# Kernel optimization log

Measured on AMD Instinct MI355X. Metric: run time of the kernel, lower is better.

Reference implementation:

```python
import jax, jax.numpy as jnp
import numpy as np
import math

N, E, B, T = 100000, 500000, 4096, 12
IN, HID, H = 64, 32, 4
HC = HID * H  # 128
ED = 4


def setup_inputs() -> dict:
    key = jax.random.key(0)
    ks = jax.random.split(key, 40)
    w = lambda k, shape: jax.random.normal(k, shape, jnp.float32) * 0.05
    inp = {
        'x': jax.random.normal(ks[0], (N, IN), jnp.float32),
        'edge_index': jax.random.randint(ks[1], (2, E), 0, N, jnp.int32),
        'edge_attr': jax.random.normal(ks[2], (E, ED), jnp.float32),
        'batch': jnp.sort(jax.random.randint(ks[3], (N,), 0, B, jnp.int32)),
        'r_target': jax.random.randint(ks[4], (B,), 0, T, jnp.int32),
        # layer 1 (in=IN)
        'Wq1': w(ks[5], (IN, HC)), 'bq1': w(ks[6], (HC,)),
        'Wk1': w(ks[7], (IN, HC)), 'bk1': w(ks[8], (HC,)),
        'Wv1': w(ks[9], (IN, HC)), 'bv1': w(ks[10], (HC,)),
        'We1': w(ks[11], (ED, HC)),
        'Ws1': w(ks[12], (IN, HC)), 'bs1': w(ks[13], (HC,)),
        # layers 2 and 3 stacked (in=HC)
        'Wq23': w(ks[14], (2, HC, HC)), 'bq23': w(ks[15], (2, HC)),
        'Wk23': w(ks[16], (2, HC, HC)), 'bk23': w(ks[17], (2, HC)),
        'Wv23': w(ks[18], (2, HC, HC)), 'bv23': w(ks[19], (2, HC)),
        'We23': w(ks[20], (2, ED, HC)),
        'Ws23': w(ks[21], (2, HC, HC)), 'bs23': w(ks[22], (2, HC)),
        # per-task linear heads (out_channels=1)
        'head_W': w(ks[23], (T, HC)), 'head_b': w(ks[24], (T,)),
    }
    return inp


def tconv(x, src, dst, ea, Wq, bq, Wk, bk, Wv, bv, We, Ws, bs):
    """PyG TransformerConv: gather -> per-edge MHA score -> segment softmax -> scatter."""
    q = (x @ Wq + bq).reshape(-1, H, HID)   # [N,H,C]
    k = (x @ Wk + bk).reshape(-1, H, HID)
    v = (x @ Wv + bv).reshape(-1, H, HID)
    e = (ea @ We).reshape(-1, H, HID)       # [E,H,C] (lin_edge has no bias)
    kj = k[src] + e                          # [E,H,C]
    alpha = (q[dst] * kj).sum(-1) / math.sqrt(HID)          # [E,H]
    amax = jax.ops.segment_max(alpha, dst, num_segments=N)  # [N,H]
    alpha = jnp.exp(alpha - amax[dst])
    asum = jax.ops.segment_sum(alpha, dst, num_segments=N)
    alpha = alpha / (asum[dst] + 1e-16)
    msg = (v[src] + e) * alpha[..., None]                   # [E,H,C]
    out = jax.ops.segment_sum(msg, dst, num_segments=N).reshape(N, HC)
    return out + x @ Ws + bs                 # root_weight skip connection


def reference(x, edge_index, edge_attr, batch, r_target,
              Wq1, bq1, Wk1, bk1, Wv1, bv1, We1, Ws1, bs1,
              Wq23, bq23, Wk23, bk23, Wv23, bv23, We23, Ws23, bs23,
              head_W, head_b):
    src, dst = edge_index[0], edge_index[1]
    h = jax.nn.relu(tconv(x, src, dst, edge_attr, Wq1, bq1, Wk1, bk1, Wv1, bv1, We1, Ws1, bs1))
    h = jax.nn.relu(tconv(h, src, dst, edge_attr, Wq23[0], bq23[0], Wk23[0], bk23[0], Wv23[0], bv23[0], We23[0], Ws23[0], bs23[0]))
    h = tconv(h, src, dst, edge_attr, Wq23[1], bq23[1], Wk23[1], bk23[1], Wv23[1], bv23[1], We23[1], Ws23[1], bs23[1])
    # global mean pool per graph
    cnt = jax.ops.segment_sum(jnp.ones((N,), h.dtype), batch, num_segments=B)
    pooled = jax.ops.segment_sum(h, batch, num_segments=B) / jnp.maximum(cnt, 1.0)[:, None]  # [B,HC]
    # dropout p=0.3 is a no-op in eval mode
    # per-task head selected by r_target (out_channels=1, squeezed)
    return (pooled * head_W[r_target]).sum(-1) + head_b[r_target]  # [B]
```

## Files before the change

kernel.cpp:

```cpp
#include <hip/hip_runtime.h>
#include <hip/hip_bf16.h>

#define NN 100000
#define EE 500000
#define BB 4096
#define HC 128
#define SCAN_ELEM 1024
#define NSB ((NN + SCAN_ELEM - 1) / SCAN_ELEM)

typedef __bf16 bf16_t;
typedef bf16_t bf16x8 __attribute__((ext_vector_type(8)));
typedef float f32x4 __attribute__((ext_vector_type(4)));

__device__ __forceinline__ unsigned short f2bf(float f) {
    unsigned u = __builtin_bit_cast(unsigned, f);
    u += 0x7FFFu + ((u >> 16) & 1u);
    return (unsigned short)(u >> 16);
}
__device__ __forceinline__ float bflo(unsigned u) {
    return __builtin_bit_cast(float, u << 16);
}
__device__ __forceinline__ float bfhi(unsigned u) {
    return __builtin_bit_cast(float, u & 0xFFFF0000u);
}

__global__ __launch_bounds__(256) void conv_x(const float* __restrict__ in,
                                              unsigned short* __restrict__ outb,
                                              int total4)
{
    const int g = blockIdx.x * 256 + threadIdx.x;
    if (g >= total4) return;
    const float4 f = *(const float4*)(in + (size_t)g * 4);
    ushort4 u;
    u.x = f2bf(f.x); u.y = f2bf(f.y); u.z = f2bf(f.z); u.w = f2bf(f.w);
    *(ushort4*)(outb + (size_t)g * 4) = u;
}

__global__ __launch_bounds__(256) void prep_w(
    const float* __restrict__ Wq, const float* __restrict__ Wk,
    const float* __restrict__ Wv, const float* __restrict__ Ws,
    unsigned short* __restrict__ Wt, int K)
{
    const int g = blockIdx.x * 256 + threadIdx.x;
    const int per = K * 128;
    if (g >= 4 * per) return;
    const int p = g / per, r = g - p * per;
    const int k = r >> 7, n = r & 127;
    const float* W = p == 0 ? Wq : p == 1 ? Wk : p == 2 ? Wv : Ws;
    Wt[(size_t)p * per + (size_t)n * K + k] = f2bf(W[k * 128 + n]);
}

template<int NKT>
__global__ __launch_bounds__(256) void gemm_mfma(
    const unsigned short* __restrict__ A,
    const unsigned short* __restrict__ Wt,
    const float* __restrict__ bq, const float* __restrict__ bk,
    const float* __restrict__ bv, const float* __restrict__ bs,
    unsigned* __restrict__ Qb, unsigned* __restrict__ Kb,
    unsigned* __restrict__ Vb, unsigned* __restrict__ Sb)
{
    constexpr int K = NKT * 32;
    const int lane = threadIdx.x & 63;
    const int p = threadIdx.x >> 6;
    const int m = lane & 15, kq = lane >> 4;
    const int rows0 = blockIdx.x * 32;

    const unsigned short* Wp = Wt + (size_t)p * 128 * K;
    const float* bias = p == 0 ? bq : p == 1 ? bk : p == 2 ? bv : bs;
    unsigned* out = p == 0 ? Qb : p == 1 ? Kb : p == 2 ? Vb : Sb;

    bf16x8 a[2][NKT];
#pragma unroll
    for (int mt = 0; mt < 2; mt++)
#pragma unroll
        for (int kt = 0; kt < NKT; kt++)
            a[mt][kt] = *(const bf16x8*)(A + (size_t)(rows0 + mt * 16 + m) * K + kt * 32 + kq * 8);

    f32x4 acc[2][8];
#pragma unroll
    for (int mt = 0; mt < 2; mt++)
#pragma unroll
        for (int nt = 0; nt < 8; nt++)
            acc[mt][nt] = (f32x4){0.f, 0.f, 0.f, 0.f};

#pragma unroll
    for (int nt = 0; nt < 8; nt++) {
#pragma unroll
        for (int kt = 0; kt < NKT; kt++) {
            const bf16x8 b = *(const bf16x8*)(Wp + (size_t)(nt * 16 + m) * K + kt * 32 + kq * 8);
            acc[0][nt] = __builtin_amdgcn_mfma_f32_16x16x32_bf16(a[0][kt], b, acc[0][nt], 0, 0, 0);
            acc[1][nt] = __builtin_amdgcn_mfma_f32_16x16x32_bf16(a[1][kt], b, acc[1][nt], 0, 0, 0);
        }
    }

#pragma unroll
    for (int nt = 0; nt < 8; nt++) {
        const float bi = bias[nt * 16 + m];
#pragma unroll
        for (int mt = 0; mt < 2; mt++) {
#pragma unroll
            for (int r = 0; r < 4; r++) {
                const float v0 = acc[mt][nt][r] + bi;
                const float v1 = __shfl_xor(v0, 1);
                if (!(m & 1)) {
                    const unsigned pk = (unsigned)f2bf(v0) | ((unsigned)f2bf(v1) << 16);
                    out[(size_t)(rows0 + mt * 16 + kq * 4 + r) * 64 + nt * 8 + (m >> 1)] = pk;
                }
            }
        }
    }
}

__global__ __launch_bounds__(256) void deg_k(const int* __restrict__ ei, int* __restrict__ deg)
{
    const int e = blockIdx.x * 256 + threadIdx.x;
    if (e < EE) atomicAdd(&deg[ei[EE + e]], 1);
}

__global__ __launch_bounds__(256) void scan_part(const int* __restrict__ deg,
                                                 int* __restrict__ bsum)
{
    __shared__ int red[256];
    const int base = blockIdx.x * SCAN_ELEM + threadIdx.x * 4;
    int s = 0;
#pragma unroll
    for (int j = 0; j < 4; j++) { const int i = base + j; if (i < NN) s += deg[i]; }
    red[threadIdx.x] = s;
    __syncthreads();
    for (int st = 128; st > 0; st >>= 1) {
        if (threadIdx.x < st) red[threadIdx.x] += red[threadIdx.x + st];
        __syncthreads();
    }
    if (threadIdx.x == 0) bsum[blockIdx.x] = red[0];
}

__global__ __launch_bounds__(128) void scan_top(const int* __restrict__ bsum,
                                                int* __restrict__ boff)
{
    __shared__ int buf[128];
    const int v = (threadIdx.x < NSB) ? bsum[threadIdx.x] : 0;
    buf[threadIdx.x] = v;
    __syncthreads();
    for (int s = 1; s < 128; s <<= 1) {
        const int t = (threadIdx.x >= s) ? buf[threadIdx.x - s] : 0;
        __syncthreads();
        buf[threadIdx.x] += t;
        __syncthreads();
    }
    if (threadIdx.x < NSB) boff[threadIdx.x] = buf[threadIdx.x] - v;
}

__global__ __launch_bounds__(256) void scan_final(const int* __restrict__ deg,
                                                  const int* __restrict__ boff,
                                                  int* __restrict__ off,
                                                  int* __restrict__ cursor)
{
    __shared__ int tsum[256];
    const int base = blockIdx.x * SCAN_ELEM + threadIdx.x * 4;
    int vals[4];
    int s = 0;
#pragma unroll
    for (int j = 0; j < 4; j++) {
        const int i = base + j;
        vals[j] = (i < NN) ? deg[i] : 0;
        s += vals[j];
    }
    tsum[threadIdx.x] = s;
    __syncthreads();
    for (int st = 1; st < 256; st <<= 1) {
        const int t = (threadIdx.x >= st) ? tsum[threadIdx.x - st] : 0;
        __syncthreads();
        tsum[threadIdx.x] += t;
        __syncthreads();
    }
    int ex = boff[blockIdx.x] + tsum[threadIdx.x] - s;
#pragma unroll
    for (int j = 0; j < 4; j++) {
        const int i = base + j;
        if (i < NN) { off[i] = ex; cursor[i] = ex; }
        ex += vals[j];
    }
    if (blockIdx.x == NSB - 1 && threadIdx.x == 255)
        off[NN] = boff[blockIdx.x] + tsum[255];
}

__global__ __launch_bounds__(256) void bucket_k(const int* __restrict__ ei,
                                                const float* __restrict__ ea,
                                                int* __restrict__ cursor,
                                                int* __restrict__ esrc,
                                                float4* __restrict__ eaf)
{
    const int e = blockIdx.x * 256 + threadIdx.x;
    if (e < EE) {
        const int d = ei[EE + e];
        const int p = atomicAdd(&cursor[d], 1);
        esrc[p] = ei[e];
        eaf[p] = *(const float4*)(ea + (size_t)e * 4);
    }
}

__global__ __launch_bounds__(256) void cnt_k(const int* __restrict__ batch,
                                             float* __restrict__ cnt)
{
    const int n = blockIdx.x * 256 + threadIdx.x;
    if (n < NN) atomicAdd(&cnt[batch[n]], 1.0f);
}

__global__ __launch_bounds__(256) void edge_fused(
    const int* __restrict__ esrc, const float4* __restrict__ eaf,
    const float* __restrict__ We,
    const unsigned* __restrict__ Qb, const unsigned* __restrict__ Kb,
    const unsigned* __restrict__ Vb,
    const int* __restrict__ off, const unsigned* __restrict__ Sb,
    unsigned short* __restrict__ Hb,
    const int* __restrict__ batch, float* __restrict__ pooled,
    int fuse_pool)
{
    __shared__ float wes[512];
    for (int i = threadIdx.x; i < 512; i += 256) wes[i] = We[i];
    __syncthreads();

    const int lane = threadIdx.x & 63;
    const int n = blockIdx.x * 4 + (threadIdx.x >> 6);
    const int c = lane * 2;
    const float w00 = wes[c],     w10 = wes[128 + c],     w20 = wes[256 + c],     w30 = wes[384 + c];
    const float w01 = wes[c + 1], w11 = wes[128 + c + 1], w21 = wes[256 + c + 1], w31 = wes[384 + c + 1];

    const int beg = off[n], end = off[n + 1];
    const unsigned qu = Qb[(size_t)n * 64 + lane];
    const float q0 = bflo(qu), q1 = bfhi(qu);
    float num0 = 0.f, num1 = 0.f, den = 0.f;

    int src = 0;
    float4 a4 = make_float4(0.f, 0.f, 0.f, 0.f);
    if (beg < end) { src = esrc[beg]; a4 = eaf[beg]; }

    for (int p = beg; p < end; p++) {
        const unsigned ku = Kb[(size_t)src * 64 + lane];
        const unsigned vu = Vb[(size_t)src * 64 + lane];
        const float4 ac = a4;
        if (p + 1 < end) { src = esrc[p + 1]; a4 = eaf[p + 1]; }
        const float e0 = ac.x * w00 + ac.y * w10 + ac.z * w20 + ac.w * w30;
        const float e1 = ac.x * w01 + ac.y * w11 + ac.z * w21 + ac.w * w31;
        float part = q0 * (bflo(ku) + e0) + q1 * (bfhi(ku) + e1);
        part += __shfl_xor(part, 1);
        part += __shfl_xor(part, 2);
        part += __shfl_xor(part, 4);
        part += __shfl_xor(part, 8);
        const float al = expf(part * 0.17677669529663687f);
        num0 += (bflo(vu) + e0) * al;
        num1 += (bfhi(vu) + e1) * al;
        den += al;
    }

    const unsigned su = Sb[(size_t)n * 64 + lane];
    const float inv = 1.f / (den + 1e-16f);
    float o0 = num0 * inv + bflo(su);
    float o1 = num1 * inv + bfhi(su);
    if (!fuse_pool) {
        o0 = fmaxf(o0, 0.f);
        o1 = fmaxf(o1, 0.f);
        const unsigned pk = (unsigned)f2bf(o0) | ((unsigned)f2bf(o1) << 16);
        *(unsigned*)(Hb + (size_t)n * HC + c) = pk;
    } else {
        const int b = batch[n];
        atomicAdd(pooled + (size_t)b * HC + c, o0);
        atomicAdd(pooled + (size_t)b * HC + c + 1, o1);
    }
}

__global__ __launch_bounds__(256) void head_k(
    const float* __restrict__ pooled, const float* __restrict__ cnt,
    const int* __restrict__ rt, const float* __restrict__ hW,
    const float* __restrict__ hb, float* __restrict__ out)
{
    const int lane = threadIdx.x & 63;
    const int b = blockIdx.x * 4 + (threadIdx.x >> 6);
    if (b >= BB) return;
    const int t = rt[b];
    const int c = lane * 2;
    const float2 p2 = *(const float2*)(pooled + (size_t)b * HC + c);
    const float2 w2 = *(const float2*)(hW + (size_t)t * HC + c);
    float part = p2.x * w2.x + p2.y * w2.y;
    part += __shfl_xor(part, 1);
    part += __shfl_xor(part, 2);
    part += __shfl_xor(part, 4);
    part += __shfl_xor(part, 8);
    part += __shfl_xor(part, 16);
    part += __shfl_xor(part, 32);
    if (lane == 0) out[b] = part / fmaxf(cnt[b], 1.0f) + hb[t];
}

extern "C" void kernel_launch(void* const* d_in, const int* in_sizes, int n_in,
                              void* d_out, int out_size, void* d_ws, size_t ws_size,
                              hipStream_t stream) {
    const float* x      = (const float*)d_in[0];
    const int*   ei     = (const int*)d_in[1];
    const float* ea     = (const float*)d_in[2];
    const int*   batch  = (const int*)d_in[3];
    const int*   rt     = (const int*)d_in[4];

    unsigned* Qb  = (unsigned*)d_ws;
    unsigned* Kb  = Qb + 6400000;
    unsigned* Vb  = Kb + 6400000;
    unsigned* Sb  = Vb + 6400000;
    unsigned short* Abf = (unsigned short*)(Sb + 6400000);
    float4* eaf   = (float4*)(Abf + 12800000);
    unsigned short* Wt = (unsigned short*)(eaf + 500000);
    float* pooled = (float*)(Wt + 65536);
    float* cnt    = pooled + 524288;
    int*   esrc   = (int*)(cnt + 4096);
    int*   deg    = esrc + 500000;
    int*   off    = deg + 100000;
    int*   cursor = off + 100004;
    int*   bsum   = cursor + 100000;
    int*   boff   = bsum + 128;

    hipMemsetAsync(deg, 0, 100000 * sizeof(int), stream);
    deg_k<<<(EE + 255) / 256, 256, 0, stream>>>(ei, deg);
    scan_part<<<NSB, 256, 0, stream>>>(deg, bsum);
    scan_top<<<1, 128, 0, stream>>>(bsum, boff);
    scan_final<<<NSB, 256, 0, stream>>>(deg, boff, off, cursor);
    bucket_k<<<(EE + 255) / 256, 256, 0, stream>>>(ei, ea, cursor, esrc, eaf);

    hipMemsetAsync(pooled, 0, (size_t)(BB * HC + BB) * sizeof(float), stream);
    cnt_k<<<(NN + 255) / 256, 256, 0, stream>>>(batch, cnt);

    conv_x<<<(NN * 64 / 4 + 255) / 256, 256, 0, stream>>>(x, Abf, NN * 64 / 4);

    for (int l = 0; l < 3; l++) {
        const int K = (l == 0) ? 64 : 128;
        const float *Wq, *Wk, *Wv, *Wsk, *bq, *bk, *bv, *bs, *We;
        if (l == 0) {
            Wq = (const float*)d_in[5];  bq = (const float*)d_in[6];
            Wk = (const float*)d_in[7];  bk = (const float*)d_in[8];
            Wv = (const float*)d_in[9];  bv = (const float*)d_in[10];
            We = (const float*)d_in[11];
            Wsk= (const float*)d_in[12]; bs = (const float*)d_in[13];
        } else {
            const int j = l - 1;
            Wq = (const float*)d_in[14] + (size_t)j * HC * HC;  bq = (const float*)d_in[15] + j * HC;
            Wk = (const float*)d_in[16] + (size_t)j * HC * HC;  bk = (const float*)d_in[17] + j * HC;
            Wv = (const float*)d_in[18] + (size_t)j * HC * HC;  bv = (const float*)d_in[19] + j * HC;
            We = (const float*)d_in[20] + (size_t)j * 4 * HC;
            Wsk= (const float*)d_in[21] + (size_t)j * HC * HC;  bs = (const float*)d_in[22] + j * HC;
        }

        prep_w<<<(4 * K * 128 + 255) / 256, 256, 0, stream>>>(Wq, Wk, Wv, Wsk, Wt, K);
        if (K == 64)
            gemm_mfma<2><<<NN / 32, 256, 0, stream>>>(Abf, Wt, bq, bk, bv, bs, Qb, Kb, Vb, Sb);
        else
            gemm_mfma<4><<<NN / 32, 256, 0, stream>>>(Abf, Wt, bq, bk, bv, bs, Qb, Kb, Vb, Sb);
        edge_fused<<<NN / 4, 256, 0, stream>>>(esrc, eaf, We, Qb, Kb, Vb, off,
                                               Sb, Abf, batch, pooled,
                                               l == 2 ? 1 : 0);
    }

    head_k<<<BB / 4, 256, 0, stream>>>(pooled, cnt, rt,
        (const float*)d_in[23], (const float*)d_in[24], (float*)d_out);
}
```

Baseline: 689.7 us.

## Sort nodes by in-degree so edge kernel waves get balanced work

Adds a degree histogram, scan and scatter that build a per-node record (node id, edge begin, edge end), with nodes grouped by in-degree capped at 32. The edge aggregation kernel now reads its node from this degree-sorted list instead of taking nodes in index order. The aim is for the four wavefronts in a block to have similar edge counts, which cuts idle time and divergence from degree imbalance. The cost is three extra small kernels, and node ordering within each degree bin comes from atomics, so memory locality for Q loads and output writes gets worse.

```diff
diff --git a/kernel.cpp b/kernel.cpp
--- a/kernel.cpp
+++ b/kernel.cpp
@@ -199,6 +199,43 @@
     }
 }
 
+__global__ __launch_bounds__(256) void dhist_k(const int* __restrict__ deg,
+                                               int* __restrict__ hist)
+{
+    const int n = blockIdx.x * 256 + threadIdx.x;
+    if (n < NN) atomicAdd(&hist[min(deg[n], 32)], 1);
+}
+
+__global__ __launch_bounds__(64) void dscan_k(int* __restrict__ hist,
+                                              int* __restrict__ hcur)
+{
+    __shared__ int buf[64];
+    const int v = (threadIdx.x < 33) ? hist[threadIdx.x] : 0;
+    buf[threadIdx.x] = v;
+    __syncthreads();
+    for (int s = 1; s < 64; s <<= 1) {
+        const int t = (threadIdx.x >= s) ? buf[threadIdx.x - s] : 0;
+        __syncthreads();
+        buf[threadIdx.x] += t;
+        __syncthreads();
+    }
+    if (threadIdx.x < 33) hcur[threadIdx.x] = buf[threadIdx.x] - v;
+}
+
+__global__ __launch_bounds__(256) void dscat_k(const int* __restrict__ deg,
+                                               const int* __restrict__ off,
+                                               int* __restrict__ hcur,
+                                               int4* __restrict__ nodeinfo)
+{
+    const int n = blockIdx.x * 256 + threadIdx.x;
+    if (n < NN) {
+        const int d = deg[n];
+        const int p = atomicAdd(&hcur[min(d, 32)], 1);
+        const int b = off[n];
+        nodeinfo[p] = make_int4(n, b, b + d, 0);
+    }
+}
+
 __global__ __launch_bounds__(256) void cnt_k(const int* __restrict__ batch,
                                              float* __restrict__ cnt)
 {
@@ -211,7 +248,7 @@
     const float* __restrict__ We,
     const unsigned* __restrict__ Qb, const unsigned* __restrict__ Kb,
     const unsigned* __restrict__ Vb,
-    const int* __restrict__ off, const unsigned* __restrict__ Sb,
+    const int4* __restrict__ nodeinfo, const unsigned* __restrict__ Sb,
     unsigned short* __restrict__ Hb,
     const int* __restrict__ batch, float* __restrict__ pooled,
     int fuse_pool)
@@ -221,12 +258,12 @@
     __syncthreads();
 
     const int lane = threadIdx.x & 63;
-    const int n = blockIdx.x * 4 + (threadIdx.x >> 6);
+    const int4 ni = nodeinfo[blockIdx.x * 4 + (threadIdx.x >> 6)];
+    const int n = ni.x, beg = ni.y, end = ni.z;
     const int c = lane * 2;
     const float w00 = wes[c],     w10 = wes[128 + c],     w20 = wes[256 + c],     w30 = wes[384 + c];
     const float w01 = wes[c + 1], w11 = wes[128 + c + 1], w21 = wes[256 + c + 1], w31 = wes[384 + c + 1];
 
-    const int beg = off[n], end = off[n + 1];
     const unsigned qu = Qb[(size_t)n * 64 + lane];
     const float q0 = bflo(qu), q1 = bfhi(qu);
     float num0 = 0.f, num1 = 0.f, den = 0.f;
@@ -306,22 +343,29 @@
     unsigned* Sb  = Vb + 6400000;
     unsigned short* Abf = (unsigned short*)(Sb + 6400000);
     float4* eaf   = (float4*)(Abf + 12800000);
-    unsigned short* Wt = (unsigned short*)(eaf + 500000);
+    int4* nodeinfo= (int4*)(eaf + 500000);
+    unsigned short* Wt = (unsigned short*)(nodeinfo + 100000);
     float* pooled = (float*)(Wt + 65536);
     float* cnt    = pooled + 524288;
     int*   esrc   = (int*)(cnt + 4096);
     int*   deg    = esrc + 500000;
-    int*   off    = deg + 100000;
+    int*   hist   = deg + 100000;
+    int*   hcur   = hist + 64;
+    int*   off    = hcur + 64;
     int*   cursor = off + 100004;
     int*   bsum   = cursor + 100000;
     int*   boff   = bsum + 128;
 
-    hipMemsetAsync(deg, 0, 100000 * sizeof(int), stream);
+    hipMemsetAsync(deg, 0, (100000 + 64) * sizeof(int), stream);
     deg_k<<<(EE + 255) / 256, 256, 0, stream>>>(ei, deg);
     scan_part<<<NSB, 256, 0, stream>>>(deg, bsum);
     scan_top<<<1, 128, 0, stream>>>(bsum, boff);
     scan_final<<<NSB, 256, 0, stream>>>(deg, boff, off, cursor);
     bucket_k<<<(EE + 255) / 256, 256, 0, stream>>>(ei, ea, cursor, esrc, eaf);
+
+    dhist_k<<<(NN + 255) / 256, 256, 0, stream>>>(deg, hist);
+    dscan_k<<<1, 64, 0, stream>>>(hist, hcur);
+    dscat_k<<<(NN + 255) / 256, 256, 0, stream>>>(deg, off, hcur, nodeinfo);
 
     hipMemsetAsync(pooled, 0, (size_t)(BB * HC + BB) * sizeof(float), stream);
     cnt_k<<<(NN + 255) / 256, 256, 0, stream>>>(batch, cnt);
@@ -351,7 +395,7 @@
             gemm_mfma<2><<<NN / 32, 256, 0, stream>>>(Abf, Wt, bq, bk, bv, bs, Qb, Kb, Vb, Sb);
         else
             gemm_mfma<4><<<NN / 32, 256, 0, stream>>>(Abf, Wt, bq, bk, bv, bs, Qb, Kb, Vb, Sb);
-        edge_fused<<<NN / 4, 256, 0, stream>>>(esrc, eaf, We, Qb, Kb, Vb, off,
+        edge_fused<<<NN / 4, 256, 0, stream>>>(esrc, eaf, We, Qb, Kb, Vb, nodeinfo,
                                                Sb, Abf, batch, pooled,
                                                l == 2 ? 1 : 0);
     }
```

Measured after the change: 1.449 ms. +110.1%, slower.
